# Performance work log

Measured on AMD Instinct MI355X. Metric: run time of the kernel, lower is better.

The kernel has to match this reference:

```python
import jax, jax.numpy as jnp
import numpy as np

L, B, D, H, K = 1024, 64, 256, 256, 4  # nodes, batch, input dim, hidden dim, heap arity


def _build_tree_schedule():
    # Deterministic 4-ary heap tree: parent(i) = (i-1)//K; children 4i+1..4i+4.
    # First K//2 children are 'left', last K//2 are 'right'. Pad slots use index L
    # (a sentinel zero row). Levels are processed deepest-first (leaves -> root).
    depth = np.zeros(L, dtype=np.int64)
    for i in range(1, L):
        depth[i] = depth[(i - 1) // K] + 1
    n_levels = int(depth.max()) + 1
    levels = [np.where(depth == d)[0] for d in range(n_levels)]
    M = max(len(lv) for lv in levels)
    level_nodes = np.full((n_levels, M), L, dtype=np.int32)
    child_idx = np.full((n_levels, M, K), L, dtype=np.int32)
    for d, lv in enumerate(levels):
        level_nodes[d, : len(lv)] = lv
        for j, n in enumerate(lv):
            for c in range(K):
                cc = K * n + c + 1
                if cc < L:
                    child_idx[d, j, c] = cc
    return jnp.asarray(level_nodes), jnp.asarray(child_idx)


def setup_inputs() -> dict:
    key = jax.random.key(0)
    ks = jax.random.split(key, 9)
    level_nodes, child_idx = _build_tree_schedule()
    sD = 1.0 / np.sqrt(D).astype(np.float32)
    sH = 1.0 / np.sqrt(H).astype(np.float32)
    return {
        "inputs": jax.random.normal(ks[0], (L, B, D), jnp.float32),
        "level_nodes": level_nodes,
        "child_idx": child_idx,
        "W_gih": jax.random.normal(ks[1], (5 * H, D), jnp.float32) * sD,
        "b_gih": jax.random.normal(ks[2], (5 * H,), jnp.float32) * sD,
        "W_glh": jax.random.normal(ks[3], (5 * H, H), jnp.float32) * sH,
        "W_grh": jax.random.normal(ks[4], (5 * H, H), jnp.float32) * sH,
        "W_cih": jax.random.normal(ks[5], (H, D), jnp.float32) * sD,
        "b_cih": jax.random.normal(ks[6], (H,), jnp.float32) * sD,
        "W_clh": jax.random.normal(ks[7], (H, H), jnp.float32) * sH,
        "W_crh": jax.random.normal(ks[8], (H, H), jnp.float32) * sH,
    }


def _tree_gru(inputs, level_nodes, child_idx, W_gih, b_gih, W_glh, W_grh,
              W_cih, b_cih, W_clh, W_crh):
    Ln, Bn, Dn = inputs.shape
    Hn = W_cih.shape[0]
    # Sentinel zero row at index Ln for padded node/child slots.
    inp_p = jnp.concatenate([inputs, jnp.zeros((1, Bn, Dn), inputs.dtype)], axis=0)
    h = jnp.zeros((Bn, Ln + 1, Hn), inputs.dtype)
    n_levels = level_nodes.shape[0]
    half = K // 2
    for d in range(n_levels - 1, -1, -1):  # leaves first, root last
        nodes = level_nodes[d]             # [M]
        ch = child_idx[d]                  # [M, K]
        # gather + sum child hidden states per side
        left_h = h[:, ch[:, 0]] + h[:, ch[:, 1]]      # [B, M, H]
        right_h = h[:, ch[:, half]] + h[:, ch[:, half + 1]]
        x = jnp.transpose(inp_p[nodes], (1, 0, 2))    # [B, M, D]
        gates = jax.nn.sigmoid(x @ W_gih.T + b_gih + left_h @ W_glh.T + right_h @ W_grh.T)
        rl, rr, zl, zr, z = jnp.split(gates, 5, axis=-1)
        cell = jnp.tanh(x @ W_cih.T + b_cih + (rl * left_h) @ W_clh.T + (rr * right_h) @ W_crh.T)
        hidden = zl * left_h + zr * right_h + z * cell
        h = h.at[:, nodes].set(hidden)
        h = h.at[:, Ln].set(0.0)  # keep sentinel row zero (padded writes land here)
    hn = h[:, :Ln]  # [B, L, H]
    # original output order: nodes 1..L-1 then root (node 0)
    outputs = jnp.concatenate([hn[:, 1:], hn[:, :1]], axis=1)
    return outputs, hn[:, 0]


def reference(inputs, level_nodes, child_idx, W_gih, b_gih, W_glh, W_grh,
              W_cih, b_cih, W_clh, W_crh):
    return _tree_gru(inputs, level_nodes, child_idx, W_gih, b_gih, W_glh, W_grh,
                     W_cih, b_cih, W_clh, W_crh)
```

## Files before the change

kernel.cpp:

```cpp
#include <hip/hip_runtime.h>


#define L_TOT 1024

typedef __attribute__((ext_vector_type(8))) short short8;
typedef __attribute__((ext_vector_type(4))) short short4v;
typedef __attribute__((ext_vector_type(4))) float f32x4;

static __device__ __forceinline__ float bf2f(unsigned short u) {
  unsigned int x = ((unsigned int)u) << 16;
  return __builtin_bit_cast(float, x);
}
static __device__ __forceinline__ unsigned short f2bf(float f) {
  unsigned int u = __builtin_bit_cast(unsigned int, f);
  u += 0x7fffu + ((u >> 16) & 1u);
  return (unsigned short)(u >> 16);
}
static __device__ __forceinline__ float sigmf(float x) { return 1.0f / (1.0f + __expf(-x)); }
static __device__ __forceinline__ float tanhf_(float x) { return 2.0f / (1.0f + __expf(-2.0f * x)) - 1.0f; }

static __device__ __forceinline__ void bar_lgkm() {
  asm volatile("s_waitcnt lgkmcnt(0)" ::: "memory");
  __builtin_amdgcn_s_barrier();
  __builtin_amdgcn_sched_barrier(0);
}

static __device__ __forceinline__ int swz_t(int orig, int nwg) {
  int q = nwg >> 3, r = nwg & 7, x = orig & 7, s = orig >> 3;
  return (x < r ? x * (q + 1) : r * (q + 1) + (x - r) * q) + s;
}

__global__ __launch_bounds__(256) void k_pre(
    const float* __restrict__ in,
    const float* __restrict__ Wgih, const float* __restrict__ Wglh, const float* __restrict__ Wgrh,
    const float* __restrict__ Wcih, const float* __restrict__ Wclh, const float* __restrict__ Wcrh,
    unsigned short* __restrict__ xb, unsigned short* __restrict__ Wg,
    unsigned short* __restrict__ Wc, unsigned short* __restrict__ Wl,
    unsigned short* __restrict__ hb) {
  int t = blockIdx.x * 256 + threadIdx.x;
  if (t < 524288) {
    const float* s = in + (size_t)t * 8;
    short8 v;
#pragma unroll
    for (int j = 0; j < 8; ++j) v[j] = (short)f2bf(s[j]);
    *(short8*)(xb + (size_t)t * 8) = v;
  }
  const int NG = 1280 * 768;
  const int NC = 256 * 768;
  const int NL = 512 * 256;
  if (t < NG) {
    int g = t / 768, k = t % 768;
    float v = (k < 256) ? Wgih[g * 256 + k] : ((k < 512) ? Wglh[g * 256 + k - 256] : Wgrh[g * 256 + k - 512]);
    Wg[t] = f2bf(v);
  } else if (t < NG + NC) {
    int t2 = t - NG;
    int g = t2 / 768, k = t2 % 768;
    float v = (k < 256) ? Wcih[g * 256 + k] : ((k < 512) ? Wclh[g * 256 + k - 256] : Wcrh[g * 256 + k - 512]);
    Wc[t2] = f2bf(v);
  } else if (t < NG + NC + NL) {
    int t2 = t - NG - NC;
    int n = t2 >> 8, k = t2 & 255;
    int g = n >> 4;
    int hc = (g >> 1) * 16 + (n & 15);
    float v = (g & 1) ? Wcih[hc * 256 + k] : Wgih[(1024 + hc) * 256 + k];
    Wl[t2] = f2bf(v);
  }
  if (t < 16384) hb[(size_t)1024 * 16384 + t] = 0;
}

__global__ __launch_bounds__(256) void k_prep(const unsigned short* __restrict__ hb,
                                              unsigned short* __restrict__ lh,
                                              unsigned short* __restrict__ rh,
                                              int rows, int row_off, int lvl_start) {
  int t = blockIdx.x * 256 + threadIdx.x;
  if (t >= rows * 32) return;
  int r = t >> 5, k8 = (t & 31) << 3;
  int gr = row_off + r;
  int node = lvl_start + (gr >> 6);
  int b = gr & 63;
  int cb = 4 * node + 1;
  int c0 = cb, c1 = cb + 1, c2 = cb + 2, c3 = cb + 3;
  c0 = (c0 < L_TOT) ? c0 : L_TOT;
  c1 = (c1 < L_TOT) ? c1 : L_TOT;
  c2 = (c2 < L_TOT) ? c2 : L_TOT;
  c3 = (c3 < L_TOT) ? c3 : L_TOT;
  const short8 v0 = *(const short8*)(hb + (size_t)c0 * 16384 + b * 256 + k8);
  const short8 v1 = *(const short8*)(hb + (size_t)c1 * 16384 + b * 256 + k8);
  const short8 v2 = *(const short8*)(hb + (size_t)c2 * 16384 + b * 256 + k8);
  const short8 v3 = *(const short8*)(hb + (size_t)c3 * 16384 + b * 256 + k8);
  short8 ol, orr;
#pragma unroll
  for (int j = 0; j < 8; ++j) {
    ol[j] = (short)f2bf(bf2f((unsigned short)v0[j]) + bf2f((unsigned short)v1[j]));
    orr[j] = (short)f2bf(bf2f((unsigned short)v2[j]) + bf2f((unsigned short)v3[j]));
  }
  *(short8*)(lh + (size_t)r * 256 + k8) = ol;
  *(short8*)(rh + (size_t)r * 256 + k8) = orr;
}

template <int EPI>
static __device__ __forceinline__ void gemm_body(
    const float* __restrict__ Af,
    const unsigned short* __restrict__ Aseg0,
    const unsigned short* __restrict__ Aseg1,
    const unsigned short* __restrict__ Aseg2,
    const unsigned short* __restrict__ Wt, const float* __restrict__ bias,
    const float* __restrict__ bias2,
    int rows, int row_off, int lvl_start, int NT, int nwg,
    const unsigned short* __restrict__ lh, const unsigned short* __restrict__ rh,
    unsigned short* __restrict__ a2l, unsigned short* __restrict__ a2r,
    unsigned short* __restrict__ p1, unsigned short* __restrict__ p2,
    unsigned short* __restrict__ zb, unsigned short* __restrict__ hb) {
  constexpr int NKT = (EPI == 2) ? 4 : 12;
  constexpr int WSTRIDE = (EPI == 2) ? 256 : 768;
  constexpr int LR = 72;
  int t = swz_t(blockIdx.x, nwg);
  int tm = t / NT, tn = t % NT;
  const int tid = threadIdx.x, lane = tid & 63, wave = tid >> 6;
  const int wr = wave >> 1, wcl = wave & 1;

  __shared__ unsigned short As[2][128 * LR];
  __shared__ unsigned short Bs[2][128 * LR];

  f32x4 acc[2][4];
#pragma unroll
  for (int i = 0; i < 2; ++i)
#pragma unroll
    for (int j = 0; j < 4; ++j) {
      f32x4 zv = {0.f, 0.f, 0.f, 0.f};
      acc[i][j] = zv;
    }

  const unsigned short* segs[3] = {Aseg0, Aseg1, Aseg2};
  const int srow = tid >> 3;
  const int scol = (tid & 7) * 8;

  short8 rva[3][2], rvb[3][2];
  f32x4 fva[3][2][2];

  auto LOADK = [&](int kt, int s) {
    int ko = (kt & 3) * 64;
#pragma unroll
    for (int i = 0; i < 2; ++i) {
      int row = srow + i * 64;
      if (EPI == 2) {
        const float* ap = Af + (size_t)(tm * 128 + row) * 256 + ko + scol;
        fva[s][i][0] = *(const f32x4*)(ap);
        fva[s][i][1] = *(const f32x4*)(ap + 4);
      } else {
        const unsigned short* segp = segs[kt >> 2];
        rva[s][i] = *(const short8*)(segp + (size_t)(tm * 128 + row) * 256 + ko + scol);
      }
      rvb[s][i] = *(const short8*)(Wt + (size_t)(tn * 128 + row) * WSTRIDE + kt * 64 + scol);
    }
  };
  auto WRITEK = [&](int s, int buf) {
#pragma unroll
    for (int i = 0; i < 2; ++i) {
      int row = srow + i * 64;
      short8 v;
      if (EPI == 2) {
#pragma unroll
        for (int j = 0; j < 4; ++j) {
          v[j] = (short)f2bf(fva[s][i][0][j]);
          v[j + 4] = (short)f2bf(fva[s][i][1][j]);
        }
      } else {
        v = rva[s][i];
      }
      *(short8*)(&As[buf][row * LR + scol]) = v;
      *(short8*)(&Bs[buf][row * LR + scol]) = rvb[s][i];
    }
  };

  LOADK(0, 0);
  LOADK(1, 1);
  if (NKT > 2) LOADK(2, 2);
  WRITEK(0, 0);
  bar_lgkm();

#pragma unroll
  for (int kt = 0; kt < NKT; ++kt) {
    const int cur = kt & 1;
    if (kt + 1 < NKT) WRITEK((kt + 1) % 3, cur ^ 1);
    if (kt + 3 < NKT) LOADK(kt + 3, kt % 3);
#pragma unroll
    for (int kk = 0; kk < 2; ++kk) {
      short8 af[2], bf[4];
#pragma unroll
      for (int mf = 0; mf < 2; ++mf)
        af[mf] = *(const short8*)(&As[cur][(wr * 32 + mf * 16 + (lane & 15)) * LR + kk * 32 + (lane >> 4) * 8]);
#pragma unroll
      for (int nf = 0; nf < 4; ++nf)
        bf[nf] = *(const short8*)(&Bs[cur][(wcl * 64 + nf * 16 + (lane & 15)) * LR + kk * 32 + (lane >> 4) * 8]);
#pragma unroll
      for (int mf = 0; mf < 2; ++mf)
#pragma unroll
        for (int nf = 0; nf < 4; ++nf)
          acc[mf][nf] = __builtin_amdgcn_mfma_f32_16x16x32_bf16(bf[nf], af[mf], acc[mf][nf], 0, 0, 0);
    }
    if (kt + 1 < NKT) bar_lgkm();
  }

  if (EPI == 2) {
#pragma unroll
    for (int nfp = 0; nfp < 2; ++nfp) {
      int nz = nfp * 2;
      int g = tn * 8 + wcl * 4 + nz;
      int hcq = (g >> 1) * 16 + (lane >> 4) * 4;
      f32x4 bzv = *(const f32x4*)(bias + 1024 + hcq);
      f32x4 bcv = *(const f32x4*)(bias2 + hcq);
#pragma unroll
      for (int mf = 0; mf < 2; ++mf) {
        int r = tm * 128 + wr * 32 + mf * 16 + (lane & 15);
        int node = 256 + (r >> 6), b = r & 63;
        short4v hv;
#pragma unroll
        for (int j = 0; j < 4; ++j) {
          float h = sigmf(acc[mf][nz][j] + bzv[j]) * tanhf_(acc[mf][nz + 1][j] + bcv[j]);
          hv[j] = (short)f2bf(h);
        }
        *(short4v*)(hb + (size_t)node * 16384 + b * 256 + hcq) = hv;
      }
    }
    return;
  }
#pragma unroll
  for (int nf = 0; nf < 4; ++nf) {
    int colq = tn * 128 + wcl * 64 + nf * 16 + (lane >> 4) * 4;
    f32x4 bsv = *(const f32x4*)(bias + colq);
    if (EPI == 0) {
      int ck = colq >> 8;
      int gcq = colq & 255;
#pragma unroll
      for (int mf = 0; mf < 2; ++mf) {
        int r = tm * 128 + wr * 32 + mf * 16 + (lane & 15);
        if (r < rows) {
          size_t idx = (size_t)r * 256 + gcq;
          f32x4 s;
#pragma unroll
          for (int j = 0; j < 4; ++j) s[j] = sigmf(acc[mf][nf][j] + bsv[j]);
          short4v res;
          if (ck == 4) {
#pragma unroll
            for (int j = 0; j < 4; ++j) res[j] = (short)f2bf(s[j]);
            *(short4v*)(zb + idx) = res;
          } else {
            const unsigned short* src = (ck == 0 || ck == 2) ? lh : rh;
            short4v hv = *(const short4v*)(src + idx);
#pragma unroll
            for (int j = 0; j < 4; ++j) res[j] = (short)f2bf(s[j] * bf2f((unsigned short)hv[j]));
            if (ck == 0)      *(short4v*)(a2l + idx) = res;
            else if (ck == 1) *(short4v*)(a2r + idx) = res;
            else if (ck == 2) *(short4v*)(p1 + idx) = res;
            else              *(short4v*)(p2 + idx) = res;
          }
        }
      }
    } else {
#pragma unroll
      for (int mf = 0; mf < 2; ++mf) {
        int r = tm * 128 + wr * 32 + mf * 16 + (lane & 15);
        if (r < rows) {
          size_t idx = (size_t)r * 256 + colq;
          short4v p1v = *(const short4v*)(p1 + idx);
          short4v p2v = *(const short4v*)(p2 + idx);
          short4v zbv = *(const short4v*)(zb + idx);
          int gr = row_off + r;
          int node = lvl_start + (gr >> 6);
          int b = gr & 63;
          short4v hv;
#pragma unroll
          for (int j = 0; j < 4; ++j) {
            float cell = tanhf_(acc[mf][nf][j] + bsv[j]);
            float hid = bf2f((unsigned short)p1v[j]) + bf2f((unsigned short)p2v[j]) +
                        bf2f((unsigned short)zbv[j]) * cell;
            hv[j] = (short)f2bf(hid);
          }
          *(short4v*)(hb + (size_t)node * 16384 + b * 256 + colq) = hv;
        }
      }
    }
  }
}

__global__ __launch_bounds__(512, 4) void k_gates(
    const unsigned short* __restrict__ A0, const unsigned short* __restrict__ A1,
    const unsigned short* __restrict__ A2, const unsigned short* __restrict__ Wt,
    const float* __restrict__ bias, int rows, int row_off, int lvl_start, int nwg,
    const unsigned short* __restrict__ lh, const unsigned short* __restrict__ rh,
    unsigned short* __restrict__ a2l, unsigned short* __restrict__ a2r,
    unsigned short* __restrict__ p1, unsigned short* __restrict__ p2,
    unsigned short* __restrict__ zb) {
  gemm_body<0>(nullptr, A0, A1, A2, Wt, bias, nullptr, rows, row_off, lvl_start, 10, nwg,
               lh, rh, a2l, a2r, p1, p2, zb, nullptr);
}

__global__ __launch_bounds__(512, 4) void k_cell(
    const unsigned short* __restrict__ A0, const unsigned short* __restrict__ A1,
    const unsigned short* __restrict__ A2, const unsigned short* __restrict__ Wt,
    const float* __restrict__ bias, int rows, int row_off, int lvl_start, int nwg,
    const unsigned short* __restrict__ p1, const unsigned short* __restrict__ p2,
    const unsigned short* __restrict__ zb, unsigned short* __restrict__ hb) {
  gemm_body<1>(nullptr, A0, A1, A2, Wt, bias, nullptr, rows, row_off, lvl_start, 2, nwg,
               nullptr, nullptr, nullptr, nullptr, (unsigned short*)p1,
               (unsigned short*)p2, (unsigned short*)zb, hb);
}

__global__ __launch_bounds__(512, 4) void k_leaf(
    const float* __restrict__ X, const unsigned short* __restrict__ Wl,
    const float* __restrict__ bg, const float* __restrict__ bc, int nwg,
    unsigned short* __restrict__ hb) {
  gemm_body<2>(X, nullptr, nullptr, nullptr, Wl, bg, bc, 49152, 0, 0, 4, nwg,
               nullptr, nullptr, nullptr, nullptr, nullptr, nullptr, nullptr, hb);
}

__global__ __launch_bounds__(256) void k_write_out(const unsigned short* __restrict__ hb,
                                                   float* __restrict__ out) {
  long long t = (long long)blockIdx.x * 256 + threadIdx.x;
  long long e = t * 8;
  const long long main_n = 16777216LL;
  if (e < main_n) {
    int b = (int)(e >> 18);
    int rem = (int)(e & 262143);
    int i = rem >> 8;
    int k = rem & 255;
    int node = (i + 1) & 1023;
    short8 v = *(const short8*)(hb + (size_t)node * 16384 + b * 256 + k);
    float4 o0, o1;
    o0.x = bf2f((unsigned short)v[0]); o0.y = bf2f((unsigned short)v[1]);
    o0.z = bf2f((unsigned short)v[2]); o0.w = bf2f((unsigned short)v[3]);
    o1.x = bf2f((unsigned short)v[4]); o1.y = bf2f((unsigned short)v[5]);
    o1.z = bf2f((unsigned short)v[6]); o1.w = bf2f((unsigned short)v[7]);
    *(float4*)(out + e) = o0;
    *(float4*)(out + e + 4) = o1;
  } else if (e < main_n + 16384) {
    int e2 = (int)(e - main_n);
    int b = e2 >> 8, k = e2 & 255;
    short8 v = *(const short8*)(hb + (size_t)b * 256 + k);
    float4 o0, o1;
    o0.x = bf2f((unsigned short)v[0]); o0.y = bf2f((unsigned short)v[1]);
    o0.z = bf2f((unsigned short)v[2]); o0.w = bf2f((unsigned short)v[3]);
    o1.x = bf2f((unsigned short)v[4]); o1.y = bf2f((unsigned short)v[5]);
    o1.z = bf2f((unsigned short)v[6]); o1.w = bf2f((unsigned short)v[7]);
    *(float4*)(out + e) = o0;
    *(float4*)(out + e + 4) = o1;
  }
}

extern "C" void kernel_launch(void* const* d_in, const int* in_sizes, int n_in,
                              void* d_out, int out_size, void* d_ws, size_t ws_size,
                              hipStream_t stream) {
  const float* inputs = (const float*)d_in[0];
  const float* W_gih = (const float*)d_in[3];
  const float* b_gih = (const float*)d_in[4];
  const float* W_glh = (const float*)d_in[5];
  const float* W_grh = (const float*)d_in[6];
  const float* W_cih = (const float*)d_in[7];
  const float* b_cih = (const float*)d_in[8];
  const float* W_clh = (const float*)d_in[9];
  const float* W_crh = (const float*)d_in[10];
  float* out = (float*)d_out;

  char* ws = (char*)d_ws;
  size_t cur = 0;
  auto alloc = [&](size_t bytes) -> char* {
    char* p = ws + cur;
    cur += (bytes + 255) & ~(size_t)255;
    return p;
  };

  unsigned short* xb = (unsigned short*)alloc((size_t)(16384 + 128) * 256 * 2);
  unsigned short* hb = (unsigned short*)alloc((size_t)1025 * 16384 * 2);
  unsigned short* Wg = (unsigned short*)alloc((size_t)1280 * 768 * 2);
  unsigned short* Wc = (unsigned short*)alloc((size_t)256 * 768 * 2);
  unsigned short* Wl = (unsigned short*)alloc((size_t)512 * 256 * 2);

  size_t rem = (ws_size > cur) ? (ws_size - cur) : 0;
  long long rcap = (long long)(rem / (7 * 512 + 64));
  rcap = (rcap / 128) * 128;
  int Rchunk = (int)((rcap < 11008) ? rcap : 11008);
  if (Rchunk < 128) Rchunk = 128;

  unsigned short* lh  = (unsigned short*)alloc((size_t)Rchunk * 512);
  unsigned short* rh  = (unsigned short*)alloc((size_t)Rchunk * 512);
  unsigned short* a2l = (unsigned short*)alloc((size_t)Rchunk * 512);
  unsigned short* a2r = (unsigned short*)alloc((size_t)Rchunk * 512);
  unsigned short* p1  = (unsigned short*)alloc((size_t)Rchunk * 512);
  unsigned short* p2  = (unsigned short*)alloc((size_t)Rchunk * 512);
  unsigned short* zb  = (unsigned short*)alloc((size_t)Rchunk * 512);

  k_pre<<<5120, 256, 0, stream>>>(inputs, W_gih, W_glh, W_grh, W_cih, W_clh, W_crh,
                                  xb, Wg, Wc, Wl, hb);

  k_leaf<<<1536, 512, 0, stream>>>(inputs + (size_t)16384 * 256, Wl, b_gih, b_cih, 1536, hb);

  static const int LSi[5] = {0, 1, 5, 21, 85};
  static const int LCi[5] = {1, 4, 16, 64, 171};

  for (int d = 4; d >= 0; --d) {
    int rows_lvl = LCi[d] * 64;
    for (int off = 0; off < rows_lvl; off += Rchunk) {
      int rows = rows_lvl - off;
      if (rows > Rchunk) rows = Rchunk;
      int tmn = (rows + 127) / 128;
      int pgrid = (rows * 32 + 255) / 256;
      k_prep<<<pgrid, 256, 0, stream>>>(hb, lh, rh, rows, off, LSi[d]);
      const unsigned short* xseg = xb + (size_t)(LSi[d] * 64 + off) * 256;
      int nwg_g = tmn * 10;
      k_gates<<<nwg_g, 512, 0, stream>>>(xseg, lh, rh, Wg, b_gih, rows, off, LSi[d], nwg_g,
                                         lh, rh, a2l, a2r, p1, p2, zb);
      int nwg_c = tmn * 2;
      k_cell<<<nwg_c, 512, 0, stream>>>(xseg, a2l, a2r, Wc, b_cih, rows, off, LSi[d], nwg_c,
                                        p1, p2, zb, hb);
    }
  }

  k_write_out<<<8200, 256, 0, stream>>>(hb, out);
}
```

Before: 262.3 us.

## Fuse fp32 output writes into epilogues and load A fragments directly from global

```diff
diff --git a/kernel.cpp b/kernel.cpp
--- a/kernel.cpp
+++ b/kernel.cpp
@@ -99,27 +99,24 @@
 }
 
 template <int EPI>
-static __device__ __forceinline__ void gemm_body(
-    const float* __restrict__ Af,
+static __device__ __forceinline__ void gemm_adirect(
     const unsigned short* __restrict__ Aseg0,
     const unsigned short* __restrict__ Aseg1,
     const unsigned short* __restrict__ Aseg2,
     const unsigned short* __restrict__ Wt, const float* __restrict__ bias,
-    const float* __restrict__ bias2,
     int rows, int row_off, int lvl_start, int NT, int nwg,
     const unsigned short* __restrict__ lh, const unsigned short* __restrict__ rh,
     unsigned short* __restrict__ a2l, unsigned short* __restrict__ a2r,
     unsigned short* __restrict__ p1, unsigned short* __restrict__ p2,
-    unsigned short* __restrict__ zb, unsigned short* __restrict__ hb) {
-  constexpr int NKT = (EPI == 2) ? 4 : 12;
-  constexpr int WSTRIDE = (EPI == 2) ? 256 : 768;
+    unsigned short* __restrict__ zb, unsigned short* __restrict__ hb,
+    float* __restrict__ out) {
+  constexpr int NKT = 12;
   constexpr int LR = 72;
   int t = swz_t(blockIdx.x, nwg);
   int tm = t / NT, tn = t % NT;
   const int tid = threadIdx.x, lane = tid & 63, wave = tid >> 6;
   const int wr = wave >> 1, wcl = wave & 1;
 
-  __shared__ unsigned short As[2][128 * LR];
   __shared__ unsigned short Bs[2][128 * LR];
 
   f32x4 acc[2][4];
@@ -135,61 +132,48 @@
   const int srow = tid >> 3;
   const int scol = (tid & 7) * 8;
 
-  short8 rva[3][2], rvb[3][2];
-  f32x4 fva[3][2][2];
-
-  auto LOADK = [&](int kt, int s) {
-    int ko = (kt & 3) * 64;
-#pragma unroll
-    for (int i = 0; i < 2; ++i) {
-      int row = srow + i * 64;
-      if (EPI == 2) {
-        const float* ap = Af + (size_t)(tm * 128 + row) * 256 + ko + scol;
-        fva[s][i][0] = *(const f32x4*)(ap);
-        fva[s][i][1] = *(const f32x4*)(ap + 4);
-      } else {
-        const unsigned short* segp = segs[kt >> 2];
-        rva[s][i] = *(const short8*)(segp + (size_t)(tm * 128 + row) * 256 + ko + scol);
-      }
-      rvb[s][i] = *(const short8*)(Wt + (size_t)(tn * 128 + row) * WSTRIDE + kt * 64 + scol);
-    }
-  };
-  auto WRITEK = [&](int s, int buf) {
-#pragma unroll
-    for (int i = 0; i < 2; ++i) {
-      int row = srow + i * 64;
-      short8 v;
-      if (EPI == 2) {
-#pragma unroll
-        for (int j = 0; j < 4; ++j) {
-          v[j] = (short)f2bf(fva[s][i][0][j]);
-          v[j + 4] = (short)f2bf(fva[s][i][1][j]);
-        }
-      } else {
-        v = rva[s][i];
-      }
-      *(short8*)(&As[buf][row * LR + scol]) = v;
-      *(short8*)(&Bs[buf][row * LR + scol]) = rvb[s][i];
-    }
-  };
-
-  LOADK(0, 0);
-  LOADK(1, 1);
-  if (NKT > 2) LOADK(2, 2);
-  WRITEK(0, 0);
+  short8 rvb[3][2];
+  short8 afr[2][2][2];
+
+  const size_t arow_base = (size_t)(tm * 128 + wr * 32 + (lane & 15)) * 256;
+  const int acol = (lane >> 4) * 8;
+
+  auto LOADA = [&](int kt, int s) {
+    const unsigned short* segp = segs[kt >> 2];
+    int ko = (kt & 3) * 64 + acol;
+#pragma unroll
+    for (int mf = 0; mf < 2; ++mf)
+#pragma unroll
+      for (int kk = 0; kk < 2; ++kk)
+        afr[s][mf][kk] = *(const short8*)(segp + arow_base + (size_t)mf * 16 * 256 + ko + kk * 32);
+  };
+  auto LOADB = [&](int kt, int s) {
+#pragma unroll
+    for (int i = 0; i < 2; ++i)
+      rvb[s][i] = *(const short8*)(Wt + (size_t)(tn * 128 + srow + i * 64) * 768 + kt * 64 + scol);
+  };
+  auto WRITEB = [&](int s, int buf) {
+#pragma unroll
+    for (int i = 0; i < 2; ++i)
+      *(short8*)(&Bs[buf][(srow + i * 64) * LR + scol]) = rvb[s][i];
+  };
+
+  LOADA(0, 0);
+  LOADB(0, 0);
+  LOADB(1, 1);
+  LOADB(2, 2);
+  WRITEB(0, 0);
   bar_lgkm();
 
 #pragma unroll
   for (int kt = 0; kt < NKT; ++kt) {
     const int cur = kt & 1;
-    if (kt + 1 < NKT) WRITEK((kt + 1) % 3, cur ^ 1);
-    if (kt + 3 < NKT) LOADK(kt + 3, kt % 3);
+    if (kt + 1 < NKT) LOADA(kt + 1, cur ^ 1);
+    if (kt + 1 < NKT) WRITEB((kt + 1) % 3, cur ^ 1);
+    if (kt + 3 < NKT) LOADB(kt + 3, kt % 3);
 #pragma unroll
     for (int kk = 0; kk < 2; ++kk) {
-      short8 af[2], bf[4];
-#pragma unroll
-      for (int mf = 0; mf < 2; ++mf)
-        af[mf] = *(const short8*)(&As[cur][(wr * 32 + mf * 16 + (lane & 15)) * LR + kk * 32 + (lane >> 4) * 8]);
+      short8 bf[4];
 #pragma unroll
       for (int nf = 0; nf < 4; ++nf)
         bf[nf] = *(const short8*)(&Bs[cur][(wcl * 64 + nf * 16 + (lane & 15)) * LR + kk * 32 + (lane >> 4) * 8]);
@@ -197,34 +181,11 @@
       for (int mf = 0; mf < 2; ++mf)
 #pragma unroll
         for (int nf = 0; nf < 4; ++nf)
-          acc[mf][nf] = __builtin_amdgcn_mfma_f32_16x16x32_bf16(bf[nf], af[mf], acc[mf][nf], 0, 0, 0);
+          acc[mf][nf] = __builtin_amdgcn_mfma_f32_16x16x32_bf16(bf[nf], afr[cur][mf][kk], acc[mf][nf], 0, 0, 0);
     }
     if (kt + 1 < NKT) bar_lgkm();
   }
 
-  if (EPI == 2) {
-#pragma unroll
-    for (int nfp = 0; nfp < 2; ++nfp) {
-      int nz = nfp * 2;
-      int g = tn * 8 + wcl * 4 + nz;
-      int hcq = (g >> 1) * 16 + (lane >> 4) * 4;
-      f32x4 bzv = *(const f32x4*)(bias + 1024 + hcq);
-      f32x4 bcv = *(const f32x4*)(bias2 + hcq);
-#pragma unroll
-      for (int mf = 0; mf < 2; ++mf) {
-        int r = tm * 128 + wr * 32 + mf * 16 + (lane & 15);
-        int node = 256 + (r >> 6), b = r & 63;
-        short4v hv;
-#pragma unroll
-        for (int j = 0; j < 4; ++j) {
-          float h = sigmf(acc[mf][nz][j] + bzv[j]) * tanhf_(acc[mf][nz + 1][j] + bcv[j]);
-          hv[j] = (short)f2bf(h);
-        }
-        *(short4v*)(hb + (size_t)node * 16384 + b * 256 + hcq) = hv;
-      }
-    }
-    return;
-  }
 #pragma unroll
   for (int nf = 0; nf < 4; ++nf) {
     int colq = tn * 128 + wcl * 64 + nf * 16 + (lane >> 4) * 4;
@@ -270,14 +231,22 @@
           int node = lvl_start + (gr >> 6);
           int b = gr & 63;
           short4v hv;
+          float4 ov;
+          float hidv[4];
 #pragma unroll
           for (int j = 0; j < 4; ++j) {
             float cell = tanhf_(acc[mf][nf][j] + bsv[j]);
             float hid = bf2f((unsigned short)p1v[j]) + bf2f((unsigned short)p2v[j]) +
                         bf2f((unsigned short)zbv[j]) * cell;
             hv[j] = (short)f2bf(hid);
+            hidv[j] = hid;
           }
+          ov.x = hidv[0]; ov.y = hidv[1]; ov.z = hidv[2]; ov.w = hidv[3];
           *(short4v*)(hb + (size_t)node * 16384 + b * 256 + colq) = hv;
+          int jj = node ? (node - 1) : 1023;
+          *(float4*)(out + (size_t)b * 262144 + (size_t)jj * 256 + colq) = ov;
+          if (node == 0)
+            *(float4*)(out + 16777216 + (size_t)b * 256 + colq) = ov;
         }
       }
     }
@@ -292,8 +261,8 @@
     unsigned short* __restrict__ a2l, unsigned short* __restrict__ a2r,
     unsigned short* __restrict__ p1, unsigned short* __restrict__ p2,
     unsigned short* __restrict__ zb) {
-  gemm_body<0>(nullptr, A0, A1, A2, Wt, bias, nullptr, rows, row_off, lvl_start, 10, nwg,
-               lh, rh, a2l, a2r, p1, p2, zb, nullptr);
+  gemm_adirect<0>(A0, A1, A2, Wt, bias, rows, row_off, lvl_start, 10, nwg,
+                  lh, rh, a2l, a2r, p1, p2, zb, nullptr, nullptr);
 }
 
 __global__ __launch_bounds__(512, 4) void k_cell(
@@ -301,50 +270,119 @@
     const unsigned short* __restrict__ A2, const unsigned short* __restrict__ Wt,
     const float* __restrict__ bias, int rows, int row_off, int lvl_start, int nwg,
     const unsigned short* __restrict__ p1, const unsigned short* __restrict__ p2,
-    const unsigned short* __restrict__ zb, unsigned short* __restrict__ hb) {
-  gemm_body<1>(nullptr, A0, A1, A2, Wt, bias, nullptr, rows, row_off, lvl_start, 2, nwg,
-               nullptr, nullptr, nullptr, nullptr, (unsigned short*)p1,
-               (unsigned short*)p2, (unsigned short*)zb, hb);
+    const unsigned short* __restrict__ zb, unsigned short* __restrict__ hb,
+    float* __restrict__ out) {
+  gemm_adirect<1>(A0, A1, A2, Wt, bias, rows, row_off, lvl_start, 2, nwg,
+                  nullptr, nullptr, nullptr, nullptr, (unsigned short*)p1,
+                  (unsigned short*)p2, (unsigned short*)zb, hb, out);
 }
 
 __global__ __launch_bounds__(512, 4) void k_leaf(
-    const float* __restrict__ X, const unsigned short* __restrict__ Wl,
-    const float* __restrict__ bg, const float* __restrict__ bc, int nwg,
-    unsigned short* __restrict__ hb) {
-  gemm_body<2>(X, nullptr, nullptr, nullptr, Wl, bg, bc, 49152, 0, 0, 4, nwg,
-               nullptr, nullptr, nullptr, nullptr, nullptr, nullptr, nullptr, hb);
-}
-
-__global__ __launch_bounds__(256) void k_write_out(const unsigned short* __restrict__ hb,
-                                                   float* __restrict__ out) {
-  long long t = (long long)blockIdx.x * 256 + threadIdx.x;
-  long long e = t * 8;
-  const long long main_n = 16777216LL;
-  if (e < main_n) {
-    int b = (int)(e >> 18);
-    int rem = (int)(e & 262143);
-    int i = rem >> 8;
-    int k = rem & 255;
-    int node = (i + 1) & 1023;
-    short8 v = *(const short8*)(hb + (size_t)node * 16384 + b * 256 + k);
-    float4 o0, o1;
-    o0.x = bf2f((unsigned short)v[0]); o0.y = bf2f((unsigned short)v[1]);
-    o0.z = bf2f((unsigned short)v[2]); o0.w = bf2f((unsigned short)v[3]);
-    o1.x = bf2f((unsigned short)v[4]); o1.y = bf2f((unsigned short)v[5]);
-    o1.z = bf2f((unsigned short)v[6]); o1.w = bf2f((unsigned short)v[7]);
-    *(float4*)(out + e) = o0;
-    *(float4*)(out + e + 4) = o1;
-  } else if (e < main_n + 16384) {
-    int e2 = (int)(e - main_n);
-    int b = e2 >> 8, k = e2 & 255;
-    short8 v = *(const short8*)(hb + (size_t)b * 256 + k);
-    float4 o0, o1;
-    o0.x = bf2f((unsigned short)v[0]); o0.y = bf2f((unsigned short)v[1]);
-    o0.z = bf2f((unsigned short)v[2]); o0.w = bf2f((unsigned short)v[3]);
-    o1.x = bf2f((unsigned short)v[4]); o1.y = bf2f((unsigned short)v[5]);
-    o1.z = bf2f((unsigned short)v[6]); o1.w = bf2f((unsigned short)v[7]);
-    *(float4*)(out + e) = o0;
-    *(float4*)(out + e + 4) = o1;
+    const float* __restrict__ Af, const unsigned short* __restrict__ Wt,
+    const float* __restrict__ bias, const float* __restrict__ bias2, int nwg,
+    unsigned short* __restrict__ hb, float* __restrict__ out) {
+  constexpr int NKT = 4;
+  constexpr int LR = 72;
+  int t = swz_t(blockIdx.x, nwg);
+  int tm = t / 4, tn = t % 4;
+  const int tid = threadIdx.x, lane = tid & 63, wave = tid >> 6;
+  const int wr = wave >> 1, wcl = wave & 1;
+
+  __shared__ unsigned short As[2][128 * LR];
+  __shared__ unsigned short Bs[2][128 * LR];
+
+  f32x4 acc[2][4];
+#pragma unroll
+  for (int i = 0; i < 2; ++i)
+#pragma unroll
+    for (int j = 0; j < 4; ++j) {
+      f32x4 zv = {0.f, 0.f, 0.f, 0.f};
+      acc[i][j] = zv;
+    }
+
+  const int srow = tid >> 3;
+  const int scol = (tid & 7) * 8;
+
+  short8 rvb[3][2];
+  f32x4 fva[3][2][2];
+
+  auto LOADK = [&](int kt, int s) {
+    int ko = (kt & 3) * 64;
+#pragma unroll
+    for (int i = 0; i < 2; ++i) {
+      int row = srow + i * 64;
+      const float* ap = Af + (size_t)(tm * 128 + row) * 256 + ko + scol;
+      fva[s][i][0] = *(const f32x4*)(ap);
+      fva[s][i][1] = *(const f32x4*)(ap + 4);
+      rvb[s][i] = *(const short8*)(Wt + (size_t)(tn * 128 + row) * 256 + kt * 64 + scol);
+    }
+  };
+  auto WRITEK = [&](int s, int buf) {
+#pragma unroll
+    for (int i = 0; i < 2; ++i) {
+      int row = srow + i * 64;
+      short8 v;
+#pragma unroll
+      for (int j = 0; j < 4; ++j) {
+        v[j] = (short)f2bf(fva[s][i][0][j]);
+        v[j + 4] = (short)f2bf(fva[s][i][1][j]);
+      }
+      *(short8*)(&As[buf][row * LR + scol]) = v;
+      *(short8*)(&Bs[buf][row * LR + scol]) = rvb[s][i];
+    }
+  };
+
+  LOADK(0, 0);
+  LOADK(1, 1);
+  LOADK(2, 2);
+  WRITEK(0, 0);
+  bar_lgkm();
+
+#pragma unroll
+  for (int kt = 0; kt < NKT; ++kt) {
+    const int cur = kt & 1;
+    if (kt + 1 < NKT) WRITEK((kt + 1) % 3, cur ^ 1);
+    if (kt + 3 < NKT) LOADK(kt + 3, kt % 3);
+#pragma unroll
+    for (int kk = 0; kk < 2; ++kk) {
+      short8 af[2], bf[4];
+#pragma unroll
+      for (int mf = 0; mf < 2; ++mf)
+        af[mf] = *(const short8*)(&As[cur][(wr * 32 + mf * 16 + (lane & 15)) * LR + kk * 32 + (lane >> 4) * 8]);
+#pragma unroll
+      for (int nf = 0; nf < 4; ++nf)
+        bf[nf] = *(const short8*)(&Bs[cur][(wcl * 64 + nf * 16 + (lane & 15)) * LR + kk * 32 + (lane >> 4) * 8]);
+#pragma unroll
+      for (int mf = 0; mf < 2; ++mf)
+#pragma unroll
+        for (int nf = 0; nf < 4; ++nf)
+          acc[mf][nf] = __builtin_amdgcn_mfma_f32_16x16x32_bf16(bf[nf], af[mf], acc[mf][nf], 0, 0, 0);
+    }
+    if (kt + 1 < NKT) bar_lgkm();
+  }
+
+#pragma unroll
+  for (int nfp = 0; nfp < 2; ++nfp) {
+    int nz = nfp * 2;
+    int g = tn * 8 + wcl * 4 + nz;
+    int hcq = (g >> 1) * 16 + (lane >> 4) * 4;
+    f32x4 bzv = *(const f32x4*)(bias + 1024 + hcq);
+    f32x4 bcv = *(const f32x4*)(bias2 + hcq);
+#pragma unroll
+    for (int mf = 0; mf < 2; ++mf) {
+      int r = tm * 128 + wr * 32 + mf * 16 + (lane & 15);
+      int node = 256 + (r >> 6), b = r & 63;
+      short4v hv;
+      float4 ov;
+#pragma unroll
+      for (int j = 0; j < 4; ++j) {
+        float h = sigmf(acc[mf][nz][j] + bzv[j]) * tanhf_(acc[mf][nz + 1][j] + bcv[j]);
+        hv[j] = (short)f2bf(h);
+        ((float*)&ov)[j] = h;
+      }
+      *(short4v*)(hb + (size_t)node * 16384 + b * 256 + hcq) = hv;
+      *(float4*)(out + (size_t)b * 262144 + (size_t)(node - 1) * 256 + hcq) = ov;
+    }
   }
 }
 
@@ -393,7 +431,7 @@
   k_pre<<<5120, 256, 0, stream>>>(inputs, W_gih, W_glh, W_grh, W_cih, W_clh, W_crh,
                                   xb, Wg, Wc, Wl, hb);
 
-  k_leaf<<<1536, 512, 0, stream>>>(inputs + (size_t)16384 * 256, Wl, b_gih, b_cih, 1536, hb);
+  k_leaf<<<1536, 512, 0, stream>>>(inputs + (size_t)16384 * 256, Wl, b_gih, b_cih, 1536, hb, out);
 
   static const int LSi[5] = {0, 1, 5, 21, 85};
   static const int LCi[5] = {1, 4, 16, 64, 171};
@@ -412,9 +450,7 @@
                                          lh, rh, a2l, a2r, p1, p2, zb);
       int nwg_c = tmn * 2;
       k_cell<<<nwg_c, 512, 0, stream>>>(xseg, a2l, a2r, Wc, b_cih, rows, off, LSi[d], nwg_c,
-                                        p1, p2, zb, hb);
-    }
-  }
-
-  k_write_out<<<8200, 256, 0, stream>>>(hb, out);
-}
+                                        p1, p2, zb, hb, out);
+    }
+  }
+}
```

Result: slower. 319.0 us (+21.6%).

## Stage gates/cell GEMM tiles via direct global-to-LDS loads with XOR swizzle

Applied to the files above, without the earlier changes.

```diff
diff --git a/kernel.cpp b/kernel.cpp
--- a/kernel.cpp
+++ b/kernel.cpp
@@ -19,6 +19,17 @@
 static __device__ __forceinline__ float sigmf(float x) { return 1.0f / (1.0f + __expf(-x)); }
 static __device__ __forceinline__ float tanhf_(float x) { return 2.0f / (1.0f + __expf(-2.0f * x)) - 1.0f; }
 
+static __device__ __forceinline__ void stage16(void* lds, const void* g) {
+  __builtin_amdgcn_global_load_lds(
+      (const __attribute__((address_space(1))) unsigned int*)g,
+      (__attribute__((address_space(3))) unsigned int*)lds, 16, 0, 0);
+}
+
+static __device__ __forceinline__ void bar_full() {
+  asm volatile("s_waitcnt vmcnt(0) lgkmcnt(0)" ::: "memory");
+  __builtin_amdgcn_s_barrier();
+  __builtin_amdgcn_sched_barrier(0);
+}
 static __device__ __forceinline__ void bar_lgkm() {
   asm volatile("s_waitcnt lgkmcnt(0)" ::: "memory");
   __builtin_amdgcn_s_barrier();
@@ -99,28 +110,25 @@
 }
 
 template <int EPI>
-static __device__ __forceinline__ void gemm_body(
-    const float* __restrict__ Af,
+static __device__ __forceinline__ void gemm_stg(
     const unsigned short* __restrict__ Aseg0,
     const unsigned short* __restrict__ Aseg1,
     const unsigned short* __restrict__ Aseg2,
     const unsigned short* __restrict__ Wt, const float* __restrict__ bias,
-    const float* __restrict__ bias2,
     int rows, int row_off, int lvl_start, int NT, int nwg,
     const unsigned short* __restrict__ lh, const unsigned short* __restrict__ rh,
     unsigned short* __restrict__ a2l, unsigned short* __restrict__ a2r,
     unsigned short* __restrict__ p1, unsigned short* __restrict__ p2,
     unsigned short* __restrict__ zb, unsigned short* __restrict__ hb) {
-  constexpr int NKT = (EPI == 2) ? 4 : 12;
-  constexpr int WSTRIDE = (EPI == 2) ? 256 : 768;
-  constexpr int LR = 72;
+  constexpr int NKT = 12;
+  constexpr int WSTRIDE = 768;
   int t = swz_t(blockIdx.x, nwg);
   int tm = t / NT, tn = t % NT;
   const int tid = threadIdx.x, lane = tid & 63, wave = tid >> 6;
   const int wr = wave >> 1, wcl = wave & 1;
 
-  __shared__ unsigned short As[2][128 * LR];
-  __shared__ unsigned short Bs[2][128 * LR];
+  __shared__ unsigned short As[2][128 * 64];
+  __shared__ unsigned short Bs[2][128 * 64];
 
   f32x4 acc[2][4];
 #pragma unroll
@@ -132,99 +140,51 @@
     }
 
   const unsigned short* segs[3] = {Aseg0, Aseg1, Aseg2};
-  const int srow = tid >> 3;
-  const int scol = (tid & 7) * 8;
-
-  short8 rva[3][2], rvb[3][2];
-  f32x4 fva[3][2][2];
-
-  auto LOADK = [&](int kt, int s) {
+
+  auto STAGE = [&](int kt, int buf) {
+    const unsigned short* segp = segs[kt >> 2];
     int ko = (kt & 3) * 64;
 #pragma unroll
     for (int i = 0; i < 2; ++i) {
-      int row = srow + i * 64;
-      if (EPI == 2) {
-        const float* ap = Af + (size_t)(tm * 128 + row) * 256 + ko + scol;
-        fva[s][i][0] = *(const f32x4*)(ap);
-        fva[s][i][1] = *(const f32x4*)(ap + 4);
-      } else {
-        const unsigned short* segp = segs[kt >> 2];
-        rva[s][i] = *(const short8*)(segp + (size_t)(tm * 128 + row) * 256 + ko + scol);
-      }
-      rvb[s][i] = *(const short8*)(Wt + (size_t)(tn * 128 + row) * WSTRIDE + kt * 64 + scol);
+      int c0 = wave * 128 + i * 64;
+      int c = c0 + lane;
+      int row = c >> 3;
+      int so = ((c & 7) ^ (row & 7)) * 8;
+      stage16(&As[buf][c0 * 8], segp + (size_t)(tm * 128 + row) * 256 + ko + so);
+      stage16(&Bs[buf][c0 * 8], Wt + (size_t)(tn * 128 + row) * WSTRIDE + kt * 64 + so);
     }
   };
-  auto WRITEK = [&](int s, int buf) {
-#pragma unroll
-    for (int i = 0; i < 2; ++i) {
-      int row = srow + i * 64;
-      short8 v;
-      if (EPI == 2) {
-#pragma unroll
-        for (int j = 0; j < 4; ++j) {
-          v[j] = (short)f2bf(fva[s][i][0][j]);
-          v[j + 4] = (short)f2bf(fva[s][i][1][j]);
-        }
-      } else {
-        v = rva[s][i];
-      }
-      *(short8*)(&As[buf][row * LR + scol]) = v;
-      *(short8*)(&Bs[buf][row * LR + scol]) = rvb[s][i];
-    }
-  };
-
-  LOADK(0, 0);
-  LOADK(1, 1);
-  if (NKT > 2) LOADK(2, 2);
-  WRITEK(0, 0);
-  bar_lgkm();
+
+  STAGE(0, 0);
 
 #pragma unroll
   for (int kt = 0; kt < NKT; ++kt) {
     const int cur = kt & 1;
-    if (kt + 1 < NKT) WRITEK((kt + 1) % 3, cur ^ 1);
-    if (kt + 3 < NKT) LOADK(kt + 3, kt % 3);
+    bar_full();
+    if (kt + 1 < NKT) STAGE(kt + 1, cur ^ 1);
 #pragma unroll
     for (int kk = 0; kk < 2; ++kk) {
       short8 af[2], bf[4];
 #pragma unroll
-      for (int mf = 0; mf < 2; ++mf)
-        af[mf] = *(const short8*)(&As[cur][(wr * 32 + mf * 16 + (lane & 15)) * LR + kk * 32 + (lane >> 4) * 8]);
-#pragma unroll
-      for (int nf = 0; nf < 4; ++nf)
-        bf[nf] = *(const short8*)(&Bs[cur][(wcl * 64 + nf * 16 + (lane & 15)) * LR + kk * 32 + (lane >> 4) * 8]);
+      for (int mf = 0; mf < 2; ++mf) {
+        int ra = wr * 32 + mf * 16 + (lane & 15);
+        int sl = (kk * 4 + (lane >> 4)) ^ (ra & 7);
+        af[mf] = *(const short8*)(&As[cur][ra * 64 + sl * 8]);
+      }
+#pragma unroll
+      for (int nf = 0; nf < 4; ++nf) {
+        int rb = wcl * 64 + nf * 16 + (lane & 15);
+        int sl = (kk * 4 + (lane >> 4)) ^ (rb & 7);
+        bf[nf] = *(const short8*)(&Bs[cur][rb * 64 + sl * 8]);
+      }
 #pragma unroll
       for (int mf = 0; mf < 2; ++mf)
 #pragma unroll
         for (int nf = 0; nf < 4; ++nf)
           acc[mf][nf] = __builtin_amdgcn_mfma_f32_16x16x32_bf16(bf[nf], af[mf], acc[mf][nf], 0, 0, 0);
     }
-    if (kt + 1 < NKT) bar_lgkm();
-  }
-
-  if (EPI == 2) {
-#pragma unroll
-    for (int nfp = 0; nfp < 2; ++nfp) {
-      int nz = nfp * 2;
-      int g = tn * 8 + wcl * 4 + nz;
-      int hcq = (g >> 1) * 16 + (lane >> 4) * 4;
-      f32x4 bzv = *(const f32x4*)(bias + 1024 + hcq);
-      f32x4 bcv = *(const f32x4*)(bias2 + hcq);
-#pragma unroll
-      for (int mf = 0; mf < 2; ++mf) {
-        int r = tm * 128 + wr * 32 + mf * 16 + (lane & 15);
-        int node = 256 + (r >> 6), b = r & 63;
-        short4v hv;
-#pragma unroll
-        for (int j = 0; j < 4; ++j) {
-          float h = sigmf(acc[mf][nz][j] + bzv[j]) * tanhf_(acc[mf][nz + 1][j] + bcv[j]);
-          hv[j] = (short)f2bf(h);
-        }
-        *(short4v*)(hb + (size_t)node * 16384 + b * 256 + hcq) = hv;
-      }
-    }
-    return;
-  }
+  }
+
 #pragma unroll
   for (int nf = 0; nf < 4; ++nf) {
     int colq = tn * 128 + wcl * 64 + nf * 16 + (lane >> 4) * 4;
@@ -292,8 +252,8 @@
     unsigned short* __restrict__ a2l, unsigned short* __restrict__ a2r,
     unsigned short* __restrict__ p1, unsigned short* __restrict__ p2,
     unsigned short* __restrict__ zb) {
-  gemm_body<0>(nullptr, A0, A1, A2, Wt, bias, nullptr, rows, row_off, lvl_start, 10, nwg,
-               lh, rh, a2l, a2r, p1, p2, zb, nullptr);
+  gemm_stg<0>(A0, A1, A2, Wt, bias, rows, row_off, lvl_start, 10, nwg,
+              lh, rh, a2l, a2r, p1, p2, zb, nullptr);
 }
 
 __global__ __launch_bounds__(512, 4) void k_cell(
@@ -302,17 +262,115 @@
     const float* __restrict__ bias, int rows, int row_off, int lvl_start, int nwg,
     const unsigned short* __restrict__ p1, const unsigned short* __restrict__ p2,
     const unsigned short* __restrict__ zb, unsigned short* __restrict__ hb) {
-  gemm_body<1>(nullptr, A0, A1, A2, Wt, bias, nullptr, rows, row_off, lvl_start, 2, nwg,
-               nullptr, nullptr, nullptr, nullptr, (unsigned short*)p1,
-               (unsigned short*)p2, (unsigned short*)zb, hb);
+  gemm_stg<1>(A0, A1, A2, Wt, bias, rows, row_off, lvl_start, 2, nwg,
+              nullptr, nullptr, nullptr, nullptr, (unsigned short*)p1,
+              (unsigned short*)p2, (unsigned short*)zb, hb);
 }
 
 __global__ __launch_bounds__(512, 4) void k_leaf(
-    const float* __restrict__ X, const unsigned short* __restrict__ Wl,
-    const float* __restrict__ bg, const float* __restrict__ bc, int nwg,
+    const float* __restrict__ Af, const unsigned short* __restrict__ Wt,
+    const float* __restrict__ bias, const float* __restrict__ bias2, int nwg,
     unsigned short* __restrict__ hb) {
-  gemm_body<2>(X, nullptr, nullptr, nullptr, Wl, bg, bc, 49152, 0, 0, 4, nwg,
-               nullptr, nullptr, nullptr, nullptr, nullptr, nullptr, nullptr, hb);
+  constexpr int NKT = 4;
+  constexpr int LR = 72;
+  int t = swz_t(blockIdx.x, nwg);
+  int tm = t / 4, tn = t % 4;
+  const int tid = threadIdx.x, lane = tid & 63, wave = tid >> 6;
+  const int wr = wave >> 1, wcl = wave & 1;
+
+  __shared__ unsigned short As[2][128 * LR];
+  __shared__ unsigned short Bs[2][128 * LR];
+
+  f32x4 acc[2][4];
+#pragma unroll
+  for (int i = 0; i < 2; ++i)
+#pragma unroll
+    for (int j = 0; j < 4; ++j) {
+      f32x4 zv = {0.f, 0.f, 0.f, 0.f};
+      acc[i][j] = zv;
+    }
+
+  const int srow = tid >> 3;
+  const int scol = (tid & 7) * 8;
+
+  short8 rvb[3][2];
+  f32x4 fva[3][2][2];
+
+  auto LOADK = [&](int kt, int s) {
+    int ko = (kt & 3) * 64;
+#pragma unroll
+    for (int i = 0; i < 2; ++i) {
+      int row = srow + i * 64;
+      const float* ap = Af + (size_t)(tm * 128 + row) * 256 + ko + scol;
+      fva[s][i][0] = *(const f32x4*)(ap);
+      fva[s][i][1] = *(const f32x4*)(ap + 4);
+      rvb[s][i] = *(const short8*)(Wt + (size_t)(tn * 128 + row) * 256 + kt * 64 + scol);
+    }
+  };
+  auto WRITEK = [&](int s, int buf) {
+#pragma unroll
+    for (int i = 0; i < 2; ++i) {
+      int row = srow + i * 64;
+      short8 v;
+#pragma unroll
+      for (int j = 0; j < 4; ++j) {
+        v[j] = (short)f2bf(fva[s][i][0][j]);
+        v[j + 4] = (short)f2bf(fva[s][i][1][j]);
+      }
+      *(short8*)(&As[buf][row * LR + scol]) = v;
+      *(short8*)(&Bs[buf][row * LR + scol]) = rvb[s][i];
+    }
+  };
+
+  LOADK(0, 0);
+  LOADK(1, 1);
+  LOADK(2, 2);
+  WRITEK(0, 0);
+  bar_lgkm();
+
+#pragma unroll
+  for (int kt = 0; kt < NKT; ++kt) {
+    const int cur = kt & 1;
+    if (kt + 1 < NKT) WRITEK((kt + 1) % 3, cur ^ 1);
+    if (kt + 3 < NKT) LOADK(kt + 3, kt % 3);
+#pragma unroll
+    for (int kk = 0; kk < 2; ++kk) {
+      short8 af[2], bf[4];
+#pragma unroll
+      for (int mf = 0; mf < 2; ++mf)
+        af[mf] = *(const short8*)(&As[cur][(wr * 32 + mf * 16 + (lane & 15)) * LR + kk * 32 + (lane >> 4) * 8]);
+#pragma unroll
+      for (int nf = 0; nf < 4; ++nf)
+        bf[nf] = *(const short8*)(&Bs[cur][(wcl * 64 + nf * 16 + (lane & 15)) * LR + kk * 32 + (lane >> 4) * 8]);
+#pragma unroll
+      for (int mf = 0; mf < 2; ++mf)
+#pragma unroll
+        for (int nf = 0; nf < 4; ++nf)
+          acc[mf][nf] = __builtin_amdgcn_mfma_f32_16x16x32_bf16(bf[nf], af[mf], acc[mf][nf], 0, 0, 0);
+    }
+    if (kt + 1 < NKT) bar_lgkm();
+  }
+
+#pragma unroll
+  for (int nfp = 0; nfp < 2; ++nfp) {
+    int nz = nfp * 2;
+    int g = tn * 8 + wcl * 4 + nz;
+    int hcq = (g >> 1) * 16 + (lane >> 4) * 4;
+    f32x4 bzv = *(const f32x4*)(bias + 1024 + hcq);
+    f32x4 bcv = *(const f32x4*)(bias2 + hcq);
+#pragma unroll
+    for (int mf = 0; mf < 2; ++mf) {
+      int r = tm * 128 + wr * 32 + mf * 16 + (lane & 15);
+      int node = 256 + (r >> 6), b = r & 63;
+      short4v hv;
+#pragma unroll
+      for (int j = 0; j < 4; ++j) {
+        float h = sigmf(acc[mf][nz][j] + bzv[j]) * tanhf_(acc[mf][nz + 1][j] + bcv[j]);
+        hv[j] = (short)f2bf(h);
+      }
+      *(short4v*)(hb + (size_t)node * 16384 + b * 256 + hcq) = hv;
+    }
+  }
 }
 
 __global__ __launch_bounds__(256) void k_write_out(const unsigned short* __restrict__ hb,
```

Result: slower. 279.5 us (+6.6%).
